# Kernel tuning notes

Measured on AMD Instinct MI355X. Metric: run time of the kernel, lower is better.

## Reference

```python
import jax, jax.numpy as jnp
import numpy as np

EMB = 1024
HEADS = 16
HEAD_DIM = EMB // HEADS
B, S = 2, 2048
FF = 4 * EMB
EPS = 1e-5


def setup_inputs() -> dict:
    key = jax.random.key(0)
    ks = jax.random.split(key, 16)
    sc = 0.02
    return {
        "x": jax.random.normal(ks[0], (B, S, EMB), dtype=jnp.float32),
        "ln1_scale": jnp.ones((EMB,), jnp.float32),
        "ln1_shift": jnp.zeros((EMB,), jnp.float32),
        "ln2_scale": jnp.ones((EMB,), jnp.float32),
        "ln2_shift": jnp.zeros((EMB,), jnp.float32),
        "wq": jax.random.normal(ks[1], (EMB, EMB), jnp.float32) * sc,
        "bq": jnp.zeros((EMB,), jnp.float32),
        "wk": jax.random.normal(ks[2], (EMB, EMB), jnp.float32) * sc,
        "bk": jnp.zeros((EMB,), jnp.float32),
        "wv": jax.random.normal(ks[3], (EMB, EMB), jnp.float32) * sc,
        "bv": jnp.zeros((EMB,), jnp.float32),
        "wo": jax.random.normal(ks[4], (EMB, EMB), jnp.float32) * sc,
        "bo": jnp.zeros((EMB,), jnp.float32),
        "w_fc": jax.random.normal(ks[5], (EMB, FF), jnp.float32) * sc,
        "b_fc": jnp.zeros((FF,), jnp.float32),
        "w_proj": jax.random.normal(ks[6], (FF, EMB), jnp.float32) * sc,
        "b_proj": jnp.zeros((EMB,), jnp.float32),
    }


def _layernorm(x, scale, shift):
    # Faithful to source: unbiased std (ddof=1) and eps added to std, not var.
    mean = jnp.mean(x, axis=-1, keepdims=True)
    std = jnp.std(x, axis=-1, keepdims=True, ddof=1)
    return scale * ((x - mean) / (std + EPS)) + shift


def _gelu(x):
    c = jnp.sqrt(jnp.asarray(2.0 / np.pi, x.dtype))
    return 0.5 * x * (1.0 + jnp.tanh(c * (x + 0.044715 * x * x * x)))


def _attention(x, wq, bq, wk, bk, wv, bv, wo, bo):
    b, s, _ = x.shape
    q = (x @ wq + bq).reshape(b, s, HEADS, HEAD_DIM).transpose(0, 2, 1, 3)
    k = (x @ wk + bk).reshape(b, s, HEADS, HEAD_DIM).transpose(0, 2, 1, 3)
    v = (x @ wv + bv).reshape(b, s, HEADS, HEAD_DIM).transpose(0, 2, 1, 3)
    scores = jnp.einsum("bhqd,bhkd->bhqk", q, k)  # [B,H,S,S]
    causal = jnp.triu(jnp.ones((s, s), bool), k=1)
    scores = jnp.where(causal, -jnp.inf, scores)
    attn = jax.nn.softmax(scores / jnp.sqrt(jnp.asarray(HEAD_DIM, x.dtype)), axis=-1)
    ctx = jnp.einsum("bhqk,bhkd->bhqd", attn, v)
    ctx = ctx.transpose(0, 2, 1, 3).reshape(b, s, EMB)
    return ctx @ wo + bo


def reference(x, ln1_scale, ln1_shift, ln2_scale, ln2_shift,
              wq, bq, wk, bk, wv, bv, wo, bo,
              w_fc, b_fc, w_proj, b_proj):
    h = x + _attention(_layernorm(x, ln1_scale, ln1_shift), wq, bq, wk, bk, wv, bv, wo, bo)
    m = _layernorm(h, ln2_scale, ln2_shift)
    m = _gelu(m @ w_fc + b_fc) @ w_proj + b_proj
    return h + m
```

## Files before the change

### kernel.cpp

```cpp
#include <hip/hip_runtime.h>
#include <hip/hip_bf16.h>

typedef float f32x4 __attribute__((ext_vector_type(4)));
typedef __bf16 bf16x8 __attribute__((ext_vector_type(8)));

#define EMB 1024
#define FFD 4096
#define NHEAD 16
#define HD 64
#define SEQ 2048
#define MROWS 4096

__device__ __forceinline__ unsigned short f2bf(float f) {
    unsigned int x = __builtin_bit_cast(unsigned int, f);
    x += 0x7fffu + ((x >> 16) & 1u);
    return (unsigned short)(x >> 16);
}

__device__ __forceinline__ f32x4 mfma16(bf16x8 a, bf16x8 b, f32x4 c) {
    return __builtin_amdgcn_mfma_f32_16x16x32_bf16(a, b, c, 0, 0, 0);
}

__device__ __forceinline__ float gelu_f(float x) {
    float u = 0.7978845608028654f * (x + 0.044715f * x * x * x);
    float e = __expf(2.0f * u);
    float th = 1.0f - 2.0f / (e + 1.0f);
    return 0.5f * x * (1.0f + th);
}

template <int EPI>
__global__ __launch_bounds__(256) void gemm_bt(
    const unsigned short* __restrict__ A, const unsigned short* __restrict__ Bt,
    const float* __restrict__ bias,
    void* __restrict__ outp, int M, int N, int K)
{
    __shared__ unsigned short As[2][128 * 32];
    __shared__ unsigned short Bs[2][128 * 32];
    const int tid  = threadIdx.x;
    const int lane = tid & 63;
    const int wid  = tid >> 6;
    const int brow = blockIdx.y << 7;
    const int bcol = blockIdx.x << 7;
    const int wr = wid >> 1, wc = wid & 1;

    f32x4 acc[4][4];
    const f32x4 zero = {0.f, 0.f, 0.f, 0.f};
#pragma unroll
    for (int m = 0; m < 4; ++m)
#pragma unroll
        for (int n = 0; n < 4; ++n) acc[m][n] = zero;

    const int nk = K >> 5;

    auto stage = [&](int buf, int k0) {
#pragma unroll
        for (int c = 0; c < 2; ++c) {
            int idx = (wid << 10) + (c << 9) + (lane << 3);
            int row = idx >> 5;
            int c8s = (idx >> 3) & 3;
            int c8g = c8s ^ ((row >> 1) & 3);
            const unsigned short* ga = A  + (size_t)(brow + row) * K + k0 + (c8g << 3);
            const unsigned short* gb = Bt + (size_t)(bcol + row) * K + k0 + (c8g << 3);
            __builtin_amdgcn_global_load_lds(
                (const __attribute__((address_space(1))) unsigned int*)ga,
                (__attribute__((address_space(3))) unsigned int*)&As[buf][idx], 16, 0, 0);
            __builtin_amdgcn_global_load_lds(
                (const __attribute__((address_space(1))) unsigned int*)gb,
                (__attribute__((address_space(3))) unsigned int*)&Bs[buf][idx], 16, 0, 0);
        }
    };

    stage(0, 0);
    for (int kt = 0; kt < nk; ++kt) {
        __syncthreads();
        if (kt + 1 < nk) stage((kt + 1) & 1, (kt + 1) << 5);
        const unsigned short* as = As[kt & 1];
        const unsigned short* bs = Bs[kt & 1];
        const int kg = lane >> 4;
        bf16x8 afr[4], bfr[4];
#pragma unroll
        for (int m = 0; m < 4; ++m) {
            int row = (wr << 6) + (m << 4) + (lane & 15);
            int c8  = kg ^ ((row >> 1) & 3);
            afr[m] = *(const bf16x8*)&as[(row << 5) + (c8 << 3)];
        }
#pragma unroll
        for (int n = 0; n < 4; ++n) {
            int row = (wc << 6) + (n << 4) + (lane & 15);
            int c8  = kg ^ ((row >> 1) & 3);
            bfr[n] = *(const bf16x8*)&bs[(row << 5) + (c8 << 3)];
        }
#pragma unroll
        for (int m = 0; m < 4; ++m)
#pragma unroll
            for (int n = 0; n < 4; ++n)
                acc[m][n] = mfma16(afr[m], bfr[n], acc[m][n]);
        __syncthreads();
    }

#pragma unroll
    for (int m = 0; m < 4; ++m) {
#pragma unroll
        for (int n = 0; n < 4; ++n) {
            const int col = bcol + (wc << 6) + (n << 4) + (lane & 15);
            const float bv = bias[col];
#pragma unroll
            for (int r = 0; r < 4; ++r) {
                const int row = brow + (wr << 6) + (m << 4) + ((lane >> 4) << 2) + r;
                float v = acc[m][n][r] + bv;
                if (EPI == 1) v = gelu_f(v);
                ((unsigned short*)outp)[(size_t)row * N + col] = f2bf(v);
            }
        }
    }
}

__global__ __launch_bounds__(256) void gemm_bt_n64(
    const unsigned short* __restrict__ A, const unsigned short* __restrict__ Bt,
    const float* __restrict__ bias, const float* __restrict__ resid,
    float* __restrict__ outp, int M, int N, int K)
{
    __shared__ unsigned short As[2][128 * 32];
    __shared__ unsigned short Bs[2][64 * 32];
    const int tid  = threadIdx.x;
    const int lane = tid & 63;
    const int wid  = tid >> 6;
    const int brow = blockIdx.y << 7;
    const int bcol = blockIdx.x << 6;

    f32x4 acc[2][4];
    const f32x4 zero = {0.f, 0.f, 0.f, 0.f};
#pragma unroll
    for (int m = 0; m < 2; ++m)
#pragma unroll
        for (int n = 0; n < 4; ++n) acc[m][n] = zero;

    const int nk = K >> 5;

    auto stage = [&](int buf, int k0) {
#pragma unroll
        for (int c = 0; c < 2; ++c) {
            int idx = (wid << 10) + (c << 9) + (lane << 3);
            int row = idx >> 5;
            int c8g = ((idx >> 3) & 3) ^ ((row >> 1) & 3);
            const unsigned short* ga = A + (size_t)(brow + row) * K + k0 + (c8g << 3);
            __builtin_amdgcn_global_load_lds(
                (const __attribute__((address_space(1))) unsigned int*)ga,
                (__attribute__((address_space(3))) unsigned int*)&As[buf][idx], 16, 0, 0);
        }
        {
            int idx = tid << 3;
            int row = idx >> 5;
            int c8g = ((idx >> 3) & 3) ^ ((row >> 1) & 3);
            const unsigned short* gb = Bt + (size_t)(bcol + row) * K + k0 + (c8g << 3);
            __builtin_amdgcn_global_load_lds(
                (const __attribute__((address_space(1))) unsigned int*)gb,
                (__attribute__((address_space(3))) unsigned int*)&Bs[buf][idx], 16, 0, 0);
        }
    };

    stage(0, 0);
    for (int kt = 0; kt < nk; ++kt) {
        __syncthreads();
        if (kt + 1 < nk) stage((kt + 1) & 1, (kt + 1) << 5);
        const unsigned short* as = As[kt & 1];
        const unsigned short* bs = Bs[kt & 1];
        const int kg = lane >> 4;
        bf16x8 afr[2], bfr[4];
#pragma unroll
        for (int m = 0; m < 2; ++m) {
            int row = (wid << 5) + (m << 4) + (lane & 15);
            int c8  = kg ^ ((row >> 1) & 3);
            afr[m] = *(const bf16x8*)&as[(row << 5) + (c8 << 3)];
        }
#pragma unroll
        for (int n = 0; n < 4; ++n) {
            int row = (n << 4) + (lane & 15);
            int c8  = kg ^ ((row >> 1) & 3);
            bfr[n] = *(const bf16x8*)&bs[(row << 5) + (c8 << 3)];
        }
#pragma unroll
        for (int m = 0; m < 2; ++m)
#pragma unroll
            for (int n = 0; n < 4; ++n)
                acc[m][n] = mfma16(afr[m], bfr[n], acc[m][n]);
        __syncthreads();
    }

#pragma unroll
    for (int m = 0; m < 2; ++m)
#pragma unroll
        for (int n = 0; n < 4; ++n) {
            const int col = bcol + (n << 4) + (lane & 15);
            const float bv = bias[col];
#pragma unroll
            for (int r = 0; r < 4; ++r) {
                const int row = brow + (wid << 5) + (m << 4) + ((lane >> 4) << 2) + r;
                outp[(size_t)row * N + col] =
                    acc[m][n][r] + bv + resid[(size_t)row * N + col];
            }
        }
}

__global__ __launch_bounds__(256) void layernorm_k(
    const float* __restrict__ x, const float* __restrict__ sc,
    const float* __restrict__ sh, unsigned short* __restrict__ outp)
{
    const int row = blockIdx.x;
    const int tid = threadIdx.x;
    const float4 v = ((const float4*)(x + (size_t)row * EMB))[tid];
    float s  = v.x + v.y + v.z + v.w;
    float ss = v.x * v.x + v.y * v.y + v.z * v.z + v.w * v.w;
#pragma unroll
    for (int o = 32; o > 0; o >>= 1) {
        s  += __shfl_down(s, o);
        ss += __shfl_down(ss, o);
    }
    __shared__ float red[8];
    if ((tid & 63) == 0) { red[tid >> 6] = s; red[(tid >> 6) + 4] = ss; }
    __syncthreads();
    s  = red[0] + red[1] + red[2] + red[3];
    ss = red[4] + red[5] + red[6] + red[7];
    const float mean = s * (1.0f / EMB);
    const float var  = (ss - s * mean) * (1.0f / (EMB - 1));
    const float inv  = 1.0f / (sqrtf(var) + 1e-5f);
    const int c = tid << 2;
    ushort4 o4;
    o4.x = f2bf((v.x - mean) * inv * sc[c + 0] + sh[c + 0]);
    o4.y = f2bf((v.y - mean) * inv * sc[c + 1] + sh[c + 1]);
    o4.z = f2bf((v.z - mean) * inv * sc[c + 2] + sh[c + 2]);
    o4.w = f2bf((v.w - mean) * inv * sc[c + 3] + sh[c + 3]);
    ((ushort4*)(outp + (size_t)row * EMB))[tid] = o4;
}

__global__ __launch_bounds__(256) void vtrans_k(
    const unsigned short* __restrict__ qkv, unsigned short* __restrict__ vt)
{
    __shared__ unsigned short T[64 * 64];
    const int tid = threadIdx.x;
    const int st = blockIdx.x, h = blockIdx.y, b = blockIdx.z;
    const size_t rowbase = (size_t)b * SEQ;
    const unsigned short* vsrc = qkv + (rowbase + (st << 6)) * 3072 + 2 * EMB + h * 64;
#pragma unroll
    for (int it = 0; it < 2; ++it) {
        const int s  = (it << 5) + (tid >> 3);
        const int d8 = tid & 7;
        uint4 w = *(const uint4*)(vsrc + (size_t)s * 3072 + (d8 << 3));
        *(uint4*)&T[(s << 6) + ((d8 ^ (s & 7)) << 3)] = w;
    }
    __syncthreads();
    unsigned short* vdst = vt + ((size_t)(b * NHEAD + h) << 6) * SEQ + (st << 6);
#pragma unroll
    for (int it = 0; it < 2; ++it) {
        const int d  = (it << 5) + (tid >> 3);
        const int s8 = tid & 7;
        unsigned short o8[8];
#pragma unroll
        for (int j = 0; j < 8; ++j) {
            const int s = (s8 << 3) + j;
            o8[j] = T[(s << 6) + (((d >> 3) ^ (s & 7)) << 3) + (d & 7)];
        }
        *(uint4*)(vdst + (size_t)d * SEQ + (s8 << 3)) = *(const uint4*)o8;
    }
}

__global__ __launch_bounds__(256) void attn_k(
    const unsigned short* __restrict__ qkv, const unsigned short* __restrict__ vt,
    unsigned short* __restrict__ ctx)
{
    __shared__ unsigned short Ks[2][64 * 64];
    __shared__ unsigned short Vts[2][64 * 64];
    __shared__ unsigned short Ps[4][16 * 64];
    const int tid  = threadIdx.x;
    const int lane = tid & 63;
    const int wid  = tid >> 6;
    const int pairi = blockIdx.x;
    const int h  = blockIdx.y;
    const int b  = blockIdx.z;
    const size_t rowbase = (size_t)b * SEQ;
    const unsigned short* kbase = qkv + rowbase * 3072 + EMB + h * 64;
    const unsigned short* vbase = vt + ((size_t)(b * NHEAD + h) << 6) * SEQ;

    auto stage = [&](int buf, int t) {
#pragma unroll
        for (int c = 0; c < 2; ++c) {
            const int idx = (wid << 10) + (c << 9) + (lane << 3);
            {
                const int kv  = idx >> 6;
                const int d8s = ((idx >> 3) & 7) ^ (kv & 7);
                const unsigned short* g = kbase + (size_t)((t << 6) + kv) * 3072 + (d8s << 3);
                __builtin_amdgcn_global_load_lds(
                    (const __attribute__((address_space(1))) unsigned int*)g,
                    (__attribute__((address_space(3))) unsigned int*)&Ks[buf][idx], 16, 0, 0);
            }
            {
                const int d   = idx >> 6;
                const int s8s = ((idx >> 3) & 7) ^ (d & 7);
                const unsigned short* g = vbase + (size_t)d * SEQ + (t << 6) + (s8s << 3);
                __builtin_amdgcn_global_load_lds(
                    (const __attribute__((address_space(1))) unsigned int*)g,
                    (__attribute__((address_space(3))) unsigned int*)&Vts[buf][idx], 16, 0, 0);
            }
        }
    };

    const f32x4 zero = {0.f, 0.f, 0.f, 0.f};

#pragma unroll 1
    for (int pass = 0; pass < 2; ++pass) {
        const int qt = pass ? (31 - pairi) : pairi;
        const int qrow0 = (qt << 6) + (wid << 4);

        bf16x8 qf[2];
        {
            const int r = qrow0 + (lane & 15);
            const int d = (lane >> 4) << 3;
            const unsigned short* qp = qkv + (rowbase + r) * 3072 + h * 64;
            qf[0] = *(const bf16x8*)&qp[d];
            qf[1] = *(const bf16x8*)&qp[32 + d];
        }

        f32x4 accd[4];
#pragma unroll
        for (int g = 0; g < 4; ++g) accd[g] = zero;
        float mrow[4], lrow[4];
#pragma unroll
        for (int r = 0; r < 4; ++r) { mrow[r] = -__builtin_inff(); lrow[r] = 0.f; }

        stage(0, 0);
#pragma unroll 1
        for (int t = 0; t <= qt; ++t) {
            __syncthreads();
            if (t < qt) stage((t + 1) & 1, t + 1);
            const unsigned short* ks = Ks[t & 1];
            const unsigned short* vs = Vts[t & 1];

            f32x4 sg[4];
#pragma unroll
            for (int g = 0; g < 4; ++g) {
                f32x4 sv = zero;
#pragma unroll
                for (int f = 0; f < 2; ++f) {
                    const int krow = (g << 4) + (lane & 15);
                    const int cb   = (f << 5) + ((lane >> 4) << 3);
                    bf16x8 kf = *(const bf16x8*)&ks[(krow << 6) + (cb ^ ((krow & 7) << 3))];
                    sv = mfma16(qf[f], kf, sv);
                }
                sg[g] = sv * 0.125f;
            }
            if (t == qt) {
#pragma unroll
                for (int g = 0; g < 4; ++g) {
                    const int kvg = (t << 6) + (g << 4) + (lane & 15);
#pragma unroll
                    for (int r = 0; r < 4; ++r) {
                        const int qg = qrow0 + ((lane >> 4) << 2) + r;
                        if (kvg > qg) sg[g][r] = -__builtin_inff();
                    }
                }
            }
            float mx[4], rs[4];
#pragma unroll
            for (int r = 0; r < 4; ++r)
                mx[r] = fmaxf(fmaxf(sg[0][r], sg[1][r]), fmaxf(sg[2][r], sg[3][r]));
#pragma unroll
            for (int o = 1; o < 16; o <<= 1)
#pragma unroll
                for (int r = 0; r < 4; ++r)
                    mx[r] = fmaxf(mx[r], __shfl_xor(mx[r], o));
#pragma unroll
            for (int r = 0; r < 4; ++r) {
                const float mn = fmaxf(mrow[r], mx[r]);
                const float so = __expf(mrow[r] - mn);
                mrow[r] = mn;
                lrow[r] *= so;
                rs[r] = 0.f;
#pragma unroll
                for (int g = 0; g < 4; ++g) {
                    const float p = __expf(sg[g][r] - mn);
                    sg[g][r] = p;
                    rs[r] += p;
                }
#pragma unroll
                for (int g = 0; g < 4; ++g) accd[g][r] *= so;
            }
#pragma unroll
            for (int o = 1; o < 16; o <<= 1)
#pragma unroll
                for (int r = 0; r < 4; ++r)
                    rs[r] += __shfl_xor(rs[r], o);
#pragma unroll
            for (int r = 0; r < 4; ++r) lrow[r] += rs[r];

#pragma unroll
            for (int g = 0; g < 4; ++g)
#pragma unroll
                for (int r = 0; r < 4; ++r) {
                    const int prow = ((lane >> 4) << 2) + r;
                    const int pcol = (g << 4) + (lane & 15);
                    Ps[wid][(prow << 6) + (pcol ^ ((prow & 7) << 3))] = f2bf(sg[g][r]);
                }
#pragma unroll
            for (int g = 0; g < 4; ++g) {
#pragma unroll
                for (int f = 0; f < 2; ++f) {
                    const int prow = lane & 15;
                    const int pcb  = (f << 5) + ((lane >> 4) << 3);
                    bf16x8 pa = *(const bf16x8*)&Ps[wid][(prow << 6) + (pcb ^ ((prow & 7) << 3))];
                    const int vrow = (g << 4) + (lane & 15);
                    bf16x8 vb = *(const bf16x8*)&vs[(vrow << 6) + (pcb ^ ((vrow & 7) << 3))];
                    accd[g] = mfma16(pa, vb, accd[g]);
                }
            }
        }

#pragma unroll
        for (int g = 0; g < 4; ++g)
#pragma unroll
            for (int r = 0; r < 4; ++r) {
                const size_t row = rowbase + qrow0 + ((lane >> 4) << 2) + r;
                const int col = h * 64 + (g << 4) + (lane & 15);
                ctx[row * EMB + col] = f2bf(accd[g][r] / lrow[r]);
            }
        __syncthreads();
    }
}

__global__ __launch_bounds__(256) void transpose_cvt(
    const float* __restrict__ W, unsigned short* __restrict__ Wt, int K, int N)
{
    __shared__ float tbuf[32][33];
    const int n0 = blockIdx.x << 5;
    const int k0 = blockIdx.y << 5;
    const int tx = threadIdx.x & 31;
    const int ty = threadIdx.x >> 5;
#pragma unroll
    for (int j = 0; j < 32; j += 8)
        tbuf[ty + j][tx] = W[(size_t)(k0 + ty + j) * N + n0 + tx];
    __syncthreads();
#pragma unroll
    for (int j = 0; j < 32; j += 8)
        Wt[(size_t)(n0 + ty + j) * K + k0 + tx] = f2bf(tbuf[tx][ty + j]);
}

__global__ void pack_bias(const float* __restrict__ bq, const float* __restrict__ bk,
                          const float* __restrict__ bv, float* __restrict__ o)
{
    const int i = blockIdx.x * 256 + threadIdx.x;
    o[i] = (i < 1024) ? bq[i] : (i < 2048) ? bk[i - 1024] : bv[i - 2048];
}

extern "C" void kernel_launch(void* const* d_in, const int* in_sizes, int n_in,
                              void* d_out, int out_size, void* d_ws, size_t ws_size,
                              hipStream_t stream)
{
    const float* x   = (const float*)d_in[0];
    const float* l1s = (const float*)d_in[1];
    const float* l1b = (const float*)d_in[2];
    const float* l2s = (const float*)d_in[3];
    const float* l2b = (const float*)d_in[4];
    const float* wq  = (const float*)d_in[5];
    const float* bq  = (const float*)d_in[6];
    const float* wk  = (const float*)d_in[7];
    const float* bk  = (const float*)d_in[8];
    const float* wv  = (const float*)d_in[9];
    const float* bv  = (const float*)d_in[10];
    const float* wo  = (const float*)d_in[11];
    const float* bo  = (const float*)d_in[12];
    const float* wfc = (const float*)d_in[13];
    const float* bfc = (const float*)d_in[14];
    const float* wpr = (const float*)d_in[15];
    const float* bpr = (const float*)d_in[16];

    unsigned short* WtQKV = (unsigned short*)d_ws;
    unsigned short* WtO   = WtQKV + (size_t)3072 * 1024;
    unsigned short* WtFC  = WtO   + (size_t)1024 * 1024;
    unsigned short* WtPR  = WtFC  + (size_t)4096 * 1024;
    unsigned short* LN1   = WtPR  + (size_t)1024 * 4096;
    unsigned short* QKV   = LN1   + (size_t)4096 * 1024;
    unsigned short* CTX   = QKV   + (size_t)4096 * 3072;
    unsigned short* LN2   = CTX   + (size_t)4096 * 1024;
    unsigned short* Gb    = LN2   + (size_t)4096 * 1024;
    float* H    = (float*)(Gb + (size_t)4096 * 4096);
    float* BQKV = H + (size_t)4096 * 1024;
    unsigned short* VT = Gb;

    dim3 blk(256);
    transpose_cvt<<<dim3(32, 32), blk, 0, stream>>>(wq, WtQKV, 1024, 1024);
    transpose_cvt<<<dim3(32, 32), blk, 0, stream>>>(wk, WtQKV + (size_t)1024 * 1024, 1024, 1024);
    transpose_cvt<<<dim3(32, 32), blk, 0, stream>>>(wv, WtQKV + (size_t)2048 * 1024, 1024, 1024);
    transpose_cvt<<<dim3(32, 32), blk, 0, stream>>>(wo, WtO, 1024, 1024);
    transpose_cvt<<<dim3(128, 32), blk, 0, stream>>>(wfc, WtFC, 1024, 4096);
    transpose_cvt<<<dim3(32, 128), blk, 0, stream>>>(wpr, WtPR, 4096, 1024);
    pack_bias<<<dim3(12), blk, 0, stream>>>(bq, bk, bv, BQKV);

    layernorm_k<<<dim3(4096), blk, 0, stream>>>(x, l1s, l1b, LN1);
    gemm_bt<0><<<dim3(24, 32), blk, 0, stream>>>(LN1, WtQKV, BQKV, QKV, 4096, 3072, 1024);
    vtrans_k<<<dim3(32, NHEAD, 2), blk, 0, stream>>>(QKV, VT);
    attn_k<<<dim3(16, NHEAD, 2), blk, 0, stream>>>(QKV, VT, CTX);
    gemm_bt_n64<<<dim3(16, 32), blk, 0, stream>>>(CTX, WtO, bo, x, H, 4096, 1024, 1024);
    layernorm_k<<<dim3(4096), blk, 0, stream>>>(H, l2s, l2b, LN2);
    gemm_bt<1><<<dim3(32, 32), blk, 0, stream>>>(LN2, WtFC, bfc, Gb, 4096, 4096, 1024);
    gemm_bt_n64<<<dim3(16, 32), blk, 0, stream>>>(Gb, WtPR, bpr, H, (float*)d_out, 4096, 1024, 4096);
}
```

Baseline: 410.7 us.

## Transpose attention MFMA layout, lazy softmax rescale, exp2 scaling, XCD-aware block remap

Attention now computes S^T so each lane owns one query row. That removes the cross-lane row reductions, leaving only two shuffles, and allows vectorized P and context stores. The softmax scale and log2(e) are folded into Q so exp2f can be used, and the running max is only rescaled when the new max exceeds the old by more than 8. GEMM and attention blocks are remapped so neighbouring tiles land on the same XCD for L2 reuse. The lazy rescale trades some numeric headroom for fewer multiplies, and pre-scaling Q in bf16 adds rounding.

```diff
diff --git a/kernel.cpp b/kernel.cpp
--- a/kernel.cpp
+++ b/kernel.cpp
@@ -17,8 +17,19 @@
     return (unsigned short)(x >> 16);
 }
 
+__device__ __forceinline__ unsigned int pack2bf(float a, float b) {
+    return (unsigned int)f2bf(a) | ((unsigned int)f2bf(b) << 16);
+}
+
 __device__ __forceinline__ f32x4 mfma16(bf16x8 a, bf16x8 b, f32x4 c) {
     return __builtin_amdgcn_mfma_f32_16x16x32_bf16(a, b, c, 0, 0, 0);
+}
+
+__device__ __forceinline__ bf16x8 scale8(bf16x8 v, float s) {
+    bf16x8 o;
+#pragma unroll
+    for (int i = 0; i < 8; ++i) o[i] = (__bf16)((float)v[i] * s);
+    return o;
 }
 
 __device__ __forceinline__ float gelu_f(float x) {
@@ -28,6 +39,14 @@
     return 0.5f * x * (1.0f + th);
 }
 
+__device__ __forceinline__ void xcd_remap(int& bx, int& by) {
+    const int nbx = gridDim.x;
+    int id = blockIdx.x + nbx * blockIdx.y;
+    int xcd = id & 7, i = id >> 3;
+    by = (i / nbx) * 8 + xcd;
+    bx = i % nbx;
+}
+
 template <int EPI>
 __global__ __launch_bounds__(256) void gemm_bt(
     const unsigned short* __restrict__ A, const unsigned short* __restrict__ Bt,
@@ -39,8 +58,9 @@
     const int tid  = threadIdx.x;
     const int lane = tid & 63;
     const int wid  = tid >> 6;
-    const int brow = blockIdx.y << 7;
-    const int bcol = blockIdx.x << 7;
+    int bx, by; xcd_remap(bx, by);
+    const int brow = by << 7;
+    const int bcol = bx << 7;
     const int wr = wid >> 1, wc = wid & 1;
 
     f32x4 acc[4][4];
@@ -125,8 +145,9 @@
     const int tid  = threadIdx.x;
     const int lane = tid & 63;
     const int wid  = tid >> 6;
-    const int brow = blockIdx.y << 7;
-    const int bcol = blockIdx.x << 6;
+    int bx, by; xcd_remap(bx, by);
+    const int brow = by << 7;
+    const int bcol = bx << 6;
 
     f32x4 acc[2][4];
     const f32x4 zero = {0.f, 0.f, 0.f, 0.f};
@@ -274,9 +295,16 @@
     const int tid  = threadIdx.x;
     const int lane = tid & 63;
     const int wid  = tid >> 6;
-    const int pairi = blockIdx.x;
-    const int h  = blockIdx.y;
-    const int b  = blockIdx.z;
+    const int q    = lane & 15;
+    const int lg   = lane >> 4;
+
+    const int id = blockIdx.x;
+    const int xcd = id & 7, i = id >> 3;
+    const int grp = ((i >> 4) << 3) + xcd;
+    const int pairi = i & 15;
+    const int h = grp & 15;
+    const int b = grp >> 4;
+
     const size_t rowbase = (size_t)b * SEQ;
     const unsigned short* kbase = qkv + rowbase * 3072 + EMB + h * 64;
     const unsigned short* vbase = vt + ((size_t)(b * NHEAD + h) << 6) * SEQ;
@@ -305,27 +333,26 @@
     };
 
     const f32x4 zero = {0.f, 0.f, 0.f, 0.f};
+    const float QSC = 0.18033688011112042f;
 
 #pragma unroll 1
     for (int pass = 0; pass < 2; ++pass) {
         const int qt = pass ? (31 - pairi) : pairi;
         const int qrow0 = (qt << 6) + (wid << 4);
+        const int qglob = qrow0 + q;
 
         bf16x8 qf[2];
         {
-            const int r = qrow0 + (lane & 15);
-            const int d = (lane >> 4) << 3;
-            const unsigned short* qp = qkv + (rowbase + r) * 3072 + h * 64;
-            qf[0] = *(const bf16x8*)&qp[d];
-            qf[1] = *(const bf16x8*)&qp[32 + d];
+            const unsigned short* qp = qkv + (rowbase + qglob) * 3072 + h * 64;
+            qf[0] = scale8(*(const bf16x8*)&qp[(lg << 3)], QSC);
+            qf[1] = scale8(*(const bf16x8*)&qp[32 + (lg << 3)], QSC);
         }
 
         f32x4 accd[4];
 #pragma unroll
-        for (int g = 0; g < 4; ++g) accd[g] = zero;
-        float mrow[4], lrow[4];
-#pragma unroll
-        for (int r = 0; r < 4; ++r) { mrow[r] = -__builtin_inff(); lrow[r] = 0.f; }
+        for (int dg = 0; dg < 4; ++dg) accd[dg] = zero;
+        float mrow = -__builtin_inff();
+        float lrow = 0.f;
 
         stage(0, 0);
 #pragma unroll 1
@@ -341,87 +368,88 @@
                 f32x4 sv = zero;
 #pragma unroll
                 for (int f = 0; f < 2; ++f) {
-                    const int krow = (g << 4) + (lane & 15);
-                    const int cb   = (f << 5) + ((lane >> 4) << 3);
+                    const int krow = (g << 4) + q;
+                    const int cb   = (f << 5) + (lg << 3);
                     bf16x8 kf = *(const bf16x8*)&ks[(krow << 6) + (cb ^ ((krow & 7) << 3))];
-                    sv = mfma16(qf[f], kf, sv);
+                    sv = mfma16(kf, qf[f], sv);
                 }
-                sg[g] = sv * 0.125f;
+                sg[g] = sv;
             }
             if (t == qt) {
 #pragma unroll
                 for (int g = 0; g < 4; ++g) {
-                    const int kvg = (t << 6) + (g << 4) + (lane & 15);
 #pragma unroll
                     for (int r = 0; r < 4; ++r) {
-                        const int qg = qrow0 + ((lane >> 4) << 2) + r;
-                        if (kvg > qg) sg[g][r] = -__builtin_inff();
+                        const int kvg = (t << 6) + (g << 4) + (lg << 2) + r;
+                        if (kvg > qglob) sg[g][r] = -__builtin_inff();
                     }
                 }
             }
-            float mx[4], rs[4];
-#pragma unroll
-            for (int r = 0; r < 4; ++r)
-                mx[r] = fmaxf(fmaxf(sg[0][r], sg[1][r]), fmaxf(sg[2][r], sg[3][r]));
-#pragma unroll
-            for (int o = 1; o < 16; o <<= 1)
-#pragma unroll
-                for (int r = 0; r < 4; ++r)
-                    mx[r] = fmaxf(mx[r], __shfl_xor(mx[r], o));
-#pragma unroll
-            for (int r = 0; r < 4; ++r) {
-                const float mn = fmaxf(mrow[r], mx[r]);
-                const float so = __expf(mrow[r] - mn);
-                mrow[r] = mn;
-                lrow[r] *= so;
-                rs[r] = 0.f;
-#pragma unroll
-                for (int g = 0; g < 4; ++g) {
-                    const float p = __expf(sg[g][r] - mn);
-                    sg[g][r] = p;
-                    rs[r] += p;
+
+            float mx = sg[0][0];
+#pragma unroll
+            for (int g = 0; g < 4; ++g)
+#pragma unroll
+                for (int r = 0; r < 4; ++r) mx = fmaxf(mx, sg[g][r]);
+            mx = fmaxf(mx, __shfl_xor(mx, 16));
+            mx = fmaxf(mx, __shfl_xor(mx, 32));
+            if (__any(mx > mrow + 8.0f)) {
+                const float mn = fmaxf(mrow, mx);
+                const float so = exp2f(mrow - mn);
+                mrow = mn;
+                lrow *= so;
+#pragma unroll
+                for (int dg = 0; dg < 4; ++dg) accd[dg] *= so;
+            }
+            float rs = 0.f;
+#pragma unroll
+            for (int g = 0; g < 4; ++g)
+#pragma unroll
+                for (int r = 0; r < 4; ++r) {
+                    const float pv = exp2f(sg[g][r] - mrow);
+                    sg[g][r] = pv;
+                    rs += pv;
                 }
-#pragma unroll
-                for (int g = 0; g < 4; ++g) accd[g][r] *= so;
-            }
-#pragma unroll
-            for (int o = 1; o < 16; o <<= 1)
-#pragma unroll
-                for (int r = 0; r < 4; ++r)
-                    rs[r] += __shfl_xor(rs[r], o);
-#pragma unroll
-            for (int r = 0; r < 4; ++r) lrow[r] += rs[r];
-
-#pragma unroll
-            for (int g = 0; g < 4; ++g)
-#pragma unroll
-                for (int r = 0; r < 4; ++r) {
-                    const int prow = ((lane >> 4) << 2) + r;
-                    const int pcol = (g << 4) + (lane & 15);
-                    Ps[wid][(prow << 6) + (pcol ^ ((prow & 7) << 3))] = f2bf(sg[g][r]);
+            rs += __shfl_xor(rs, 16);
+            rs += __shfl_xor(rs, 32);
+            lrow += rs;
+
+#pragma unroll
+            for (int g = 0; g < 4; ++g) {
+                uint2 w;
+                w.x = pack2bf(sg[g][0], sg[g][1]);
+                w.y = pack2bf(sg[g][2], sg[g][3]);
+                const int e = ((g << 4) + (lg << 2)) ^ ((q & 7) << 3);
+                *(uint2*)&Ps[wid][(q << 6) + e] = w;
+            }
+
+            bf16x8 pa[2];
+#pragma unroll
+            for (int f = 0; f < 2; ++f) {
+                const int e = ((f << 5) + (lg << 3)) ^ ((q & 7) << 3);
+                pa[f] = *(const bf16x8*)&Ps[wid][(q << 6) + e];
+            }
+#pragma unroll
+            for (int dg = 0; dg < 4; ++dg) {
+#pragma unroll
+                for (int f = 0; f < 2; ++f) {
+                    const int vrow = (dg << 4) + q;
+                    const int cb   = (f << 5) + (lg << 3);
+                    bf16x8 vb = *(const bf16x8*)&vs[(vrow << 6) + (cb ^ ((vrow & 7) << 3))];
+                    accd[dg] = mfma16(vb, pa[f], accd[dg]);
                 }
-#pragma unroll
-            for (int g = 0; g < 4; ++g) {
-#pragma unroll
-                for (int f = 0; f < 2; ++f) {
-                    const int prow = lane & 15;
-                    const int pcb  = (f << 5) + ((lane >> 4) << 3);
-                    bf16x8 pa = *(const bf16x8*)&Ps[wid][(prow << 6) + (pcb ^ ((prow & 7) << 3))];
-                    const int vrow = (g << 4) + (lane & 15);
-                    bf16x8 vb = *(const bf16x8*)&vs[(vrow << 6) + (pcb ^ ((vrow & 7) << 3))];
-                    accd[g] = mfma16(pa, vb, accd[g]);
-                }
-            }
-        }
-
-#pragma unroll
-        for (int g = 0; g < 4; ++g)
-#pragma unroll
-            for (int r = 0; r < 4; ++r) {
-                const size_t row = rowbase + qrow0 + ((lane >> 4) << 2) + r;
-                const int col = h * 64 + (g << 4) + (lane & 15);
-                ctx[row * EMB + col] = f2bf(accd[g][r] / lrow[r]);
-            }
+            }
+        }
+
+        const float inv = 1.0f / lrow;
+        unsigned short* cp = ctx + (rowbase + qglob) * EMB + h * 64 + (lg << 2);
+#pragma unroll
+        for (int dg = 0; dg < 4; ++dg) {
+            uint2 w;
+            w.x = pack2bf(accd[dg][0] * inv, accd[dg][1] * inv);
+            w.y = pack2bf(accd[dg][2] * inv, accd[dg][3] * inv);
+            *(uint2*)(cp + (dg << 4)) = w;
+        }
         __syncthreads();
     }
 }
@@ -497,7 +525,7 @@
     layernorm_k<<<dim3(4096), blk, 0, stream>>>(x, l1s, l1b, LN1);
     gemm_bt<0><<<dim3(24, 32), blk, 0, stream>>>(LN1, WtQKV, BQKV, QKV, 4096, 3072, 1024);
     vtrans_k<<<dim3(32, NHEAD, 2), blk, 0, stream>>>(QKV, VT);
-    attn_k<<<dim3(16, NHEAD, 2), blk, 0, stream>>>(QKV, VT, CTX);
+    attn_k<<<dim3(512), blk, 0, stream>>>(QKV, VT, CTX);
     gemm_bt_n64<<<dim3(16, 32), blk, 0, stream>>>(CTX, WtO, bo, x, H, 4096, 1024, 1024);
     layernorm_k<<<dim3(4096), blk, 0, stream>>>(H, l2s, l2b, LN2);
     gemm_bt<1><<<dim3(32, 32), blk, 0, stream>>>(LN2, WtFC, bfc, Gb, 4096, 4096, 1024);
```

After: 393.0 us. -4.3%, faster.
